# Kernel tuning notes

Measured on AMD Instinct MI355X. Metric: run time of the kernel, lower is better.

Reference implementation:

```python
import jax, jax.numpy as jnp
import numpy as np


def setup_inputs() -> dict:
    key = jax.random.key(0)
    k1, k2 = jax.random.split(key)
    B, N, M, D = 4, 1024, 1024, 64
    traj1 = jax.random.normal(k1, (B, N, D), dtype=jnp.float32)
    traj2 = jax.random.normal(k2, (B, M, D), dtype=jnp.float32)
    return {"traj1": traj1, "traj2": traj2}


def reference(traj1, traj2):
    # Pairwise squared Euclidean distances: [B, N, M]
    # Faithful to sum((traj1[:, :, None] - traj2[:, None, :])**2, -1)
    diff = traj1[:, :, None, :] - traj2[:, None, :, :]  # [B, N, M, D]
    return jnp.sum(jnp.square(diff), axis=-1)
```

## Files before the change

kernel.cpp:

```cpp
#include <hip/hip_runtime.h>


#define B_ 4
#define N_ 1024
#define M_ 1024
#define D_ 64
#define BN 64
#define BM 128

typedef __attribute__((ext_vector_type(8))) __fp16 f16x8;
typedef __attribute__((ext_vector_type(2))) __fp16 f16x2;
typedef __attribute__((ext_vector_type(4))) float f32x4;

union F16x8 {
  f16x8 v;
  f16x2 h[4];
};

__device__ __forceinline__ f16x8 load_frag8(const float* __restrict__ p) {
  float4 v0 = *reinterpret_cast<const float4*>(p);
  float4 v1 = *reinterpret_cast<const float4*>(p + 4);
  F16x8 r;
  r.h[0] = __builtin_amdgcn_cvt_pkrtz(v0.x, v0.y);
  r.h[1] = __builtin_amdgcn_cvt_pkrtz(v0.z, v0.w);
  r.h[2] = __builtin_amdgcn_cvt_pkrtz(v1.x, v1.y);
  r.h[3] = __builtin_amdgcn_cvt_pkrtz(v1.z, v1.w);
  return r.v;
}

__global__ __launch_bounds__(256, 2)
void dist2_mfma(const float* __restrict__ A, const float* __restrict__ Bm,
                float* __restrict__ out) {
  __shared__ float naS[BN];
  __shared__ float nbS[BM];

  const int tid = threadIdx.x;
  const int b  = blockIdx.z;
  const int n0 = blockIdx.y * BN;
  const int m0 = blockIdx.x * BM;

  const float* Ab = A  + (size_t)b * N_ * D_;
  const float* Bb = Bm + (size_t)b * M_ * D_;

  if (tid < BN + BM) {
    const float* p = (tid < BN) ? (Ab + (size_t)(n0 + tid) * D_)
                                : (Bb + (size_t)(m0 + tid - BN) * D_);
    float s = 0.f;
    #pragma unroll
    for (int k4 = 0; k4 < D_ / 4; ++k4) {
      float4 v = *reinterpret_cast<const float4*>(p + k4 * 4);
      s = fmaf(v.x, v.x, s);
      s = fmaf(v.y, v.y, s);
      s = fmaf(v.z, v.z, s);
      s = fmaf(v.w, v.w, s);
    }
    if (tid < BN) naS[tid] = s; else nbS[tid - BN] = s;
  }

  const int wid  = tid >> 6;
  const int lane = tid & 63;
  const int wn = wid >> 1;
  const int wm = wid & 1;
  const int lr = lane & 15;
  const int kb = (lane >> 4) * 8;

  const float* An = Ab + (size_t)(n0 + wn * 32 + lr) * D_;
  const float* Bn = Bb + (size_t)(m0 + wm * 64 + lr) * D_;

  f32x4 acc[2][4];
  #pragma unroll
  for (int i = 0; i < 2; ++i)
    #pragma unroll
    for (int j = 0; j < 4; ++j) acc[i][j] = (f32x4){0.f, 0.f, 0.f, 0.f};

  #pragma unroll
  for (int ks = 0; ks < 2; ++ks) {
    const int k = ks * 32 + kb;
    f16x8 af[2], bf[4];
    #pragma unroll
    for (int nf = 0; nf < 2; ++nf) af[nf] = load_frag8(An + (size_t)nf * 16 * D_ + k);
    #pragma unroll
    for (int mf = 0; mf < 4; ++mf) bf[mf] = load_frag8(Bn + (size_t)mf * 16 * D_ + k);
    #pragma unroll
    for (int nf = 0; nf < 2; ++nf)
      #pragma unroll
      for (int mf = 0; mf < 4; ++mf)
        acc[nf][mf] = __builtin_amdgcn_mfma_f32_16x16x32_f16(bf[mf], af[nf], acc[nf][mf], 0, 0, 0);
  }

  __syncthreads();

  const int mg = (lane >> 4) * 4;

  #pragma unroll
  for (int nf = 0; nf < 2; ++nf) {
    const int nloc = wn * 32 + nf * 16 + (lane & 15);
    const float na = naS[nloc];
    float* orow = out + ((size_t)b * N_ + n0 + nloc) * M_ + m0;
    #pragma unroll
    for (int mf = 0; mf < 4; ++mf) {
      const int mloc = wm * 64 + mf * 16 + mg;
      float4 nb = *reinterpret_cast<const float4*>(&nbS[mloc]);
      f32x4 a = acc[nf][mf];
      float4 r;
      r.x = fmaf(-2.f, a[0], na + nb.x);
      r.y = fmaf(-2.f, a[1], na + nb.y);
      r.z = fmaf(-2.f, a[2], na + nb.z);
      r.w = fmaf(-2.f, a[3], na + nb.w);
      *reinterpret_cast<float4*>(orow + mloc) = r;
    }
  }
}

extern "C" void kernel_launch(void* const* d_in, const int* in_sizes, int n_in,
                              void* d_out, int out_size, void* d_ws, size_t ws_size,
                              hipStream_t stream) {
  const float* A  = (const float*)d_in[0];
  const float* Bm = (const float*)d_in[1];
  float* out = (float*)d_out;
  dim3 grid(M_ / BM, N_ / BN, B_);
  dist2_mfma<<<grid, dim3(256), 0, stream>>>(A, Bm, out);
}
```

Measured before the change: 17.70 us.

## Shrink tile to 64x64 with one 16-row strip per wave and nontemporal stores

Reduces the block tile from 64x128 to 64x64, so each wave computes a 16x64 strip with four MFMA accumulators instead of eight. Occupancy is raised to 4 blocks per SM via launch bounds and the grid doubles, giving more parallelism for this small, store-bound problem. Output writes now use nontemporal stores to avoid polluting the cache with the 16 MB result. In exchange, each block recomputes more norms and reloads more of the B rows per output element.

```diff
diff --git a/kernel.cpp b/kernel.cpp
--- a/kernel.cpp
+++ b/kernel.cpp
@@ -6,7 +6,7 @@
 #define M_ 1024
 #define D_ 64
 #define BN 64
-#define BM 128
+#define BM 64
 
 typedef __attribute__((ext_vector_type(8))) __fp16 f16x8;
 typedef __attribute__((ext_vector_type(2))) __fp16 f16x2;
@@ -28,7 +28,7 @@
   return r.v;
 }
 
-__global__ __launch_bounds__(256, 2)
+__global__ __launch_bounds__(256, 4)
 void dist2_mfma(const float* __restrict__ A, const float* __restrict__ Bm,
                 float* __restrict__ out) {
   __shared__ float naS[BN];
@@ -59,56 +59,46 @@
 
   const int wid  = tid >> 6;
   const int lane = tid & 63;
-  const int wn = wid >> 1;
-  const int wm = wid & 1;
   const int lr = lane & 15;
   const int kb = (lane >> 4) * 8;
 
-  const float* An = Ab + (size_t)(n0 + wn * 32 + lr) * D_;
-  const float* Bn = Bb + (size_t)(m0 + wm * 64 + lr) * D_;
+  const float* An = Ab + (size_t)(n0 + wid * 16 + lr) * D_;
+  const float* Bn = Bb + (size_t)(m0 + lr) * D_;
 
-  f32x4 acc[2][4];
+  f32x4 acc[4];
   #pragma unroll
-  for (int i = 0; i < 2; ++i)
-    #pragma unroll
-    for (int j = 0; j < 4; ++j) acc[i][j] = (f32x4){0.f, 0.f, 0.f, 0.f};
+  for (int j = 0; j < 4; ++j) acc[j] = (f32x4){0.f, 0.f, 0.f, 0.f};
 
   #pragma unroll
   for (int ks = 0; ks < 2; ++ks) {
     const int k = ks * 32 + kb;
-    f16x8 af[2], bf[4];
-    #pragma unroll
-    for (int nf = 0; nf < 2; ++nf) af[nf] = load_frag8(An + (size_t)nf * 16 * D_ + k);
+    f16x8 af = load_frag8(An + k);
+    f16x8 bf[4];
     #pragma unroll
     for (int mf = 0; mf < 4; ++mf) bf[mf] = load_frag8(Bn + (size_t)mf * 16 * D_ + k);
     #pragma unroll
-    for (int nf = 0; nf < 2; ++nf)
-      #pragma unroll
-      for (int mf = 0; mf < 4; ++mf)
-        acc[nf][mf] = __builtin_amdgcn_mfma_f32_16x16x32_f16(bf[mf], af[nf], acc[nf][mf], 0, 0, 0);
+    for (int mf = 0; mf < 4; ++mf)
+      acc[mf] = __builtin_amdgcn_mfma_f32_16x16x32_f16(bf[mf], af, acc[mf], 0, 0, 0);
   }
 
   __syncthreads();
 
   const int mg = (lane >> 4) * 4;
+  const int nloc = wid * 16 + (lane & 15);
+  const float na = naS[nloc];
+  float* orow = out + ((size_t)b * N_ + n0 + nloc) * M_ + m0;
 
   #pragma unroll
-  for (int nf = 0; nf < 2; ++nf) {
-    const int nloc = wn * 32 + nf * 16 + (lane & 15);
-    const float na = naS[nloc];
-    float* orow = out + ((size_t)b * N_ + n0 + nloc) * M_ + m0;
-    #pragma unroll
-    for (int mf = 0; mf < 4; ++mf) {
-      const int mloc = wm * 64 + mf * 16 + mg;
-      float4 nb = *reinterpret_cast<const float4*>(&nbS[mloc]);
-      f32x4 a = acc[nf][mf];
-      float4 r;
-      r.x = fmaf(-2.f, a[0], na + nb.x);
-      r.y = fmaf(-2.f, a[1], na + nb.y);
-      r.z = fmaf(-2.f, a[2], na + nb.z);
-      r.w = fmaf(-2.f, a[3], na + nb.w);
-      *reinterpret_cast<float4*>(orow + mloc) = r;
-    }
+  for (int mf = 0; mf < 4; ++mf) {
+    const int mloc = mf * 16 + mg;
+    f32x4 nb = *reinterpret_cast<const f32x4*>(&nbS[mloc]);
+    f32x4 a = acc[mf];
+    f32x4 r;
+    r[0] = fmaf(-2.f, a[0], na + nb[0]);
+    r[1] = fmaf(-2.f, a[1], na + nb[1]);
+    r[2] = fmaf(-2.f, a[2], na + nb[2]);
+    r[3] = fmaf(-2.f, a[3], na + nb[3]);
+    __builtin_nontemporal_store(r, reinterpret_cast<f32x4*>(orow + mloc));
   }
 }
 
```

New measurement: 20.23 us. +14.3%, slower.
